# Kernel optimization log

Measured on AMD Instinct MI355X. Metric: run time of the kernel, lower is better.

The kernel has to match this reference:

```python
import jax, jax.numpy as jnp
import numpy as np

THRESH = 64.0        # titans.surprise_threshold
NOISE_SCALE = 1e-6   # tie-breaking noise scale in _update_memory


def setup_inputs() -> dict:
    key = jax.random.key(0)
    ks = jax.random.split(key, 8)
    B, S, H, M = 2, 2048, 1024, 8192
    return {
        "hidden_states": jax.random.normal(ks[0], (B, S, H), dtype=jnp.float32),
        "memory_buffer": jax.random.normal(ks[1], (M, H), dtype=jnp.float32),
        "importance_scores": jax.random.uniform(ks[2], (M,), dtype=jnp.float32),
        "Wq": jax.random.normal(ks[3], (H, H), dtype=jnp.float32) * 0.02,
        "bq": jnp.zeros((H,), dtype=jnp.float32),
        "Wk": jax.random.normal(ks[4], (H, H), dtype=jnp.float32) * 0.02,
        "bk": jnp.zeros((H,), dtype=jnp.float32),
        "noise": jax.random.normal(ks[5], (M,), dtype=jnp.float32),
    }


def reference(hidden_states, memory_buffer, importance_scores, Wq, bq, Wk, bk, noise):
    B, S, H = hidden_states.shape
    M = memory_buffer.shape[0]

    # ---- surprise (gradient_norm method) ----
    # proxy_loss = sum((h - 0)^2)  =>  d loss / d h = 2h  =>  surprise = 2*||h||_2
    cands = hidden_states.reshape(-1, H)                      # [B*S, H]
    surprise = 2.0 * jnp.linalg.norm(cands, axis=-1)          # [B*S]

    # ---- _update_memory (torch.no_grad) ----
    # mask below-threshold candidates out, then take the (at most memory_size)
    # most surprising candidates in descending order (== argsort descending +
    # slice in the torch code; -inf entries sort last and are marked invalid).
    K = min(cands.shape[0], M)
    masked = jnp.where(surprise > THRESH, surprise, -jnp.inf)
    top_s, top_i = jax.lax.top_k(masked, K)                   # descending surprise
    valid = top_s > THRESH                                    # true only for real candidates

    # least-important memory slots (topk largest=False with tie-break noise)
    _, least_idx = jax.lax.top_k(-(importance_scores + noise * NOISE_SCALE), K)

    # scatter-write: i-th most surprising candidate -> i-th least important slot.
    # invalid lanes write to index M which is dropped (out of range).
    write_idx = jnp.where(valid, least_idx, M)                # [K]
    states_w = jax.lax.stop_gradient(cands[top_i])            # update path is no_grad
    scores_w = jax.lax.stop_gradient(jnp.where(valid, top_s, 0.0))
    new_buffer = memory_buffer.at[write_idx].set(states_w, mode="drop")   # [M, H]
    new_importance = importance_scores.at[write_idx].set(scores_w, mode="drop")
    del new_importance  # bookkeeping state; does not affect retrieved output

    # ---- query (cross-attention over memory) ----
    q = hidden_states @ Wq.T + bq                             # [B, S, H]
    mk = new_buffer @ Wk.T + bk                               # [M, H]
    scores = jnp.einsum("bsh,mh->bsm", q, mk) * (H ** -0.5)
    attn = jax.nn.softmax(scores, axis=-1)                    # [B, S, M]
    retrieved = jnp.einsum("bsm,mh->bsh", attn, new_buffer)   # [B, S, H]
    return retrieved
```

## Files before the change

### kernel.cpp

```cpp
#include <hip/hip_runtime.h>
#include <hip/hip_bf16.h>
#include <math.h>
#include <stdint.h>

typedef __attribute__((ext_vector_type(4))) float floatx4;
typedef __attribute__((ext_vector_type(8))) short shortx8;
typedef __attribute__((ext_vector_type(4))) unsigned short ushortx4;

#define BS_CAND 4096
#define HDIM    1024
#define MSLOTS  8192
#define THRESH  64.0f
#define PV_SPLIT 4
#define PS_COLS 128

__device__ __forceinline__ unsigned short f2b_bits(float f) {
    __hip_bfloat16 b = __float2bfloat16(f);
    return *(unsigned short*)&b;
}
__device__ __forceinline__ float b2f_bits(unsigned short u) {
    return __uint_as_float(((unsigned)u) << 16);
}

__device__ __forceinline__ float blockReduceSum(float x) {
    __shared__ float red[4];
    #pragma unroll
    for (int o = 32; o > 0; o >>= 1) x += __shfl_down(x, o, 64);
    int lane = threadIdx.x & 63, w = threadIdx.x >> 6;
    if (lane == 0) red[w] = x;
    __syncthreads();
    float s = red[0] + red[1] + red[2] + red[3];
    __syncthreads();
    return s;
}

__global__ __launch_bounds__(256) void pre_k(const float* __restrict__ h,
                                             float* __restrict__ sur,
                                             __hip_bfloat16* __restrict__ Hbf,
                                             const float* __restrict__ imp,
                                             const float* __restrict__ noi,
                                             float* __restrict__ keys,
                                             int* __restrict__ row_src,
                                             const float* __restrict__ Wq,
                                             __hip_bfloat16* __restrict__ Wqbf,
                                             const float* __restrict__ Wk,
                                             __hip_bfloat16* __restrict__ Wkbf) {
    int b = blockIdx.x;
    if (b < BS_CAND) {
        float4 v = ((const float4*)(h + (size_t)b * HDIM))[threadIdx.x];
        ushortx4 o;
        o.x = f2b_bits(v.x); o.y = f2b_bits(v.y);
        o.z = f2b_bits(v.z); o.w = f2b_bits(v.w);
        ((ushortx4*)(Hbf + (size_t)b * HDIM))[threadIdx.x] = o;
        float s = v.x * v.x + v.y * v.y + v.z * v.z + v.w * v.w;
        float tot = blockReduceSum(s);
        if (threadIdx.x == 0) sur[b] = 2.0f * sqrtf(tot);
    } else if (b < BS_CAND + MSLOTS / 256) {
        int i = (b - BS_CAND) * 256 + threadIdx.x;
        keys[i] = imp[i] + noi[i] * 1e-6f;
        row_src[i] = -1;
    } else {
        int w = b - (BS_CAND + MSLOTS / 256);
        const float* in = (w < 1024) ? Wq : Wk;
        __hip_bfloat16* out = (w < 1024) ? Wqbf : Wkbf;
        int j = (w & 1023) * 256 + threadIdx.x;
        float4 v = ((const float4*)in)[j];
        ushortx4 o;
        o.x = f2b_bits(v.x); o.y = f2b_bits(v.y);
        o.z = f2b_bits(v.z); o.w = f2b_bits(v.w);
        ((ushortx4*)out)[j] = o;
    }
}

__global__ __launch_bounds__(256) void ranks_k(const float* __restrict__ sur,
                                               int* __restrict__ cand_ord,
                                               const float* __restrict__ keys,
                                               int* __restrict__ slot_ord) {
    int b = blockIdx.x;
    if (b < BS_CAND) {
        float ki = sur[b];
        float cnt = 0.f;
        for (int j = threadIdx.x; j < BS_CAND; j += 256) {
            float kj = sur[j];
            cnt += ((kj > ki) || (kj == ki && j < b)) ? 1.f : 0.f;
        }
        float r = blockReduceSum(cnt);
        if (threadIdx.x == 0) cand_ord[(int)r] = b;
    } else {
        int i = b - BS_CAND;
        float ki = keys[i];
        float cnt = 0.f;
        for (int j = threadIdx.x; j < MSLOTS; j += 256) {
            float kj = keys[j];
            cnt += ((kj < ki) || (kj == ki && j < i)) ? 1.f : 0.f;
        }
        float r = blockReduceSum(cnt);
        if (threadIdx.x == 0) slot_ord[(int)r] = i;
    }
}

__global__ __launch_bounds__(256) void scatter_k(const int* __restrict__ cand_order,
                                                 const int* __restrict__ slot_order,
                                                 const float* __restrict__ sur,
                                                 int* __restrict__ row_src) {
    int i = blockIdx.x * 256 + threadIdx.x;
    int c = cand_order[i];
    if (sur[c] > THRESH) row_src[slot_order[i]] = c;
}

__global__ __launch_bounds__(256) void bbt_k(const float* __restrict__ mem,
                                             const float* __restrict__ hid,
                                             const int* __restrict__ src,
                                             __hip_bfloat16* __restrict__ B,
                                             __hip_bfloat16* __restrict__ BT) {
    __shared__ unsigned short t[64][72];
    int cb = blockIdx.x * 64, rb = blockIdx.y * 64;
    int tx = threadIdx.x & 63, ty = threadIdx.x >> 6;
    #pragma unroll
    for (int k = 0; k < 16; k++) {
        int r = ty * 16 + k;
        int s = src[rb + r];
        const float* row = (s < 0) ? (mem + (size_t)(rb + r) * HDIM)
                                   : (hid + (size_t)s * HDIM);
        unsigned short b = f2b_bits(row[cb + tx]);
        t[r][tx] = b;
        ((unsigned short*)B)[(size_t)(rb + r) * HDIM + cb + tx] = b;
    }
    __syncthreads();
    #pragma unroll
    for (int k = 0; k < 16; k++) {
        int c = ty * 16 + k;
        ((unsigned short*)BT)[(size_t)(cb + c) * MSLOTS + rb + tx] = t[tx][c];
    }
}

__device__ __forceinline__ void load_lds16(const __hip_bfloat16* g, __hip_bfloat16* l) {
    __builtin_amdgcn_global_load_lds(
        (const __attribute__((address_space(1))) void*)g,
        (__attribute__((address_space(3))) void*)l, 16, 0, 0);
}

template <int EPI, int SWAP>
__global__ __launch_bounds__(512, 2) void gemm_bt(const __hip_bfloat16* __restrict__ A,
                                                  const __hip_bfloat16* __restrict__ Bt,
                                                  const __hip_bfloat16* __restrict__ Bt2,
                                                  __hip_bfloat16* __restrict__ outH,
                                                  const float* __restrict__ bias,
                                                  const float* __restrict__ bias2,
                                                  float* __restrict__ ps,
                                                  int rows0b,
                                                  int M, int N, int K, int ksplit,
                                                  float scale) {
    extern __shared__ char lds[];
    const int tid = threadIdx.x;
    const int wave = tid >> 6, lane = tid & 63;
    const int lm = lane & 15, lq = lane >> 4;
    const int wm = wave >> 2, wn = wave & 3;
    const int bm = SWAP ? blockIdx.x : blockIdx.y;
    const int bn = SWAP ? blockIdx.y : blockIdx.x;
    const int kb = blockIdx.z * ksplit;
    const int niters = ksplit >> 7;

    const __hip_bfloat16* BtSel = (EPI == 1 && bm >= rows0b) ? Bt2 : Bt;
    const float* biasSel = (EPI == 1 && bm >= rows0b) ? bias2 : bias;

    const int l8 = lane >> 3;
    const int colsrc = ((((lane & 7) << 4) ^ (l8 << 4)) >> 1);
    const __hip_bfloat16* Abase = A + (size_t)bm * 256 * K;
    const __hip_bfloat16* Bbase = BtSel + (size_t)bn * 256 * K;
    const __hip_bfloat16* srcA[2][2];
    const __hip_bfloat16* srcB[2][2];
    #pragma unroll
    for (int h = 0; h < 2; h++)
        #pragma unroll
        for (int t = 0; t < 2; t++) {
            int row = t * 128 + h * 64 + wave * 8 + l8;
            srcA[h][t] = Abase + (size_t)row * K + colsrc;
            srcB[h][t] = Bbase + (size_t)row * K + colsrc;
        }

    const int cxor = (lq << 4) ^ ((lm & 7) << 4);
    const int a_b0 = (wm * 64 + lm) * 128 + cxor;
    const int a_b1 = a_b0 ^ 64;
    const int b_b0 = (wn * 32 + lm) * 128 + cxor;
    const int b_b1 = b_b0 ^ 64;

    floatx4 acc[8][4];
    #pragma unroll
    for (int i = 0; i < 8; i++)
        #pragma unroll
        for (int j = 0; j < 4; j++) acc[i][j] = {0.f, 0.f, 0.f, 0.f};

    shortx8 af[4][2], bf0h[2][2], bf1h[2][2];

#define LDSV(off) (*(const shortx8*)(lds + (off)))
#define READ_A(g, bo) do {                                                  \
    const int ab_ = (bo) + (g) * 16384;                                     \
    af[0][0] = LDSV(ab_ + a_b0);        af[0][1] = LDSV(ab_ + a_b1);        \
    af[1][0] = LDSV(ab_ + a_b0 + 2048); af[1][1] = LDSV(ab_ + a_b1 + 2048); \
    af[2][0] = LDSV(ab_ + a_b0 + 4096); af[2][1] = LDSV(ab_ + a_b1 + 4096); \
    af[3][0] = LDSV(ab_ + a_b0 + 6144); af[3][1] = LDSV(ab_ + a_b1 + 6144); \
} while (0)
#define READ_B(dst, g, bo) do {                                             \
    const int bb_ = (bo) + 32768 + (g) * 16384;                             \
    dst[0][0] = LDSV(bb_ + b_b0);        dst[0][1] = LDSV(bb_ + b_b1);      \
    dst[1][0] = LDSV(bb_ + b_b0 + 2048); dst[1][1] = LDSV(bb_ + b_b1 + 2048);\
} while (0)
#define STAGE(xs, h, buf, kofs) do {                                        \
    char* d_ = lds + (buf) * 65536 + (xs) * 32768 + (h) * 16384 + wave * 1024; \
    load_lds16(((xs) ? srcB : srcA)[h][0] + (kofs), (__hip_bfloat16*)d_);   \
    load_lds16(((xs) ? srcB : srcA)[h][1] + (kofs), (__hip_bfloat16*)(d_ + 8192)); \
} while (0)
#define MFQ(mh, nh, BF) do {                                                \
    __builtin_amdgcn_s_setprio(1);                                          \
    _Pragma("unroll")                                                       \
    for (int ii_ = 0; ii_ < 4; ii_++)                                       \
        _Pragma("unroll")                                                   \
        for (int jj_ = 0; jj_ < 2; jj_++) {                                 \
            acc[(mh)*4+ii_][(nh)*2+jj_] = __builtin_amdgcn_mfma_f32_16x16x32_bf16( \
                af[ii_][0], BF[jj_][0], acc[(mh)*4+ii_][(nh)*2+jj_], 0, 0, 0); \
            acc[(mh)*4+ii_][(nh)*2+jj_] = __builtin_amdgcn_mfma_f32_16x16x32_bf16( \
                af[ii_][1], BF[jj_][1], acc[(mh)*4+ii_][(nh)*2+jj_], 0, 0, 0); \
        }                                                                   \
    __builtin_amdgcn_s_setprio(0);                                          \
} while (0)
#define BAR() __builtin_amdgcn_s_barrier()
#define LGKM0() asm volatile("s_waitcnt lgkmcnt(0)" ::: "memory")
#define VMC6() asm volatile("s_waitcnt vmcnt(6)" ::: "memory")
#define VMC0() asm volatile("s_waitcnt vmcnt(0)" ::: "memory")

    STAGE(0, 0, 0, kb);
    STAGE(1, 1, 0, kb);
    STAGE(0, 1, 0, kb);
    STAGE(1, 0, 0, kb);
    STAGE(0, 0, 1, kb + 64);
    STAGE(1, 1, 1, kb + 64);
    STAGE(0, 1, 1, kb + 64);
    VMC6();
    BAR();

#define ITER(E, kcur, knext) do {                                           \
                                                                   \
    READ_A(0, 0); READ_B(bf0h, 0, 0); STAGE(1, 0, 1, (kcur) + 64);          \
    BAR(); LGKM0(); MFQ(0, 0, bf0h); BAR();                                 \
                                                                   \
    READ_B(bf1h, 1, 0); if (E) STAGE(0, 0, 0, (knext));                     \
    BAR(); LGKM0(); MFQ(0, 1, bf1h); BAR();                                 \
                                                                   \
    READ_A(1, 0); if (E) STAGE(1, 1, 0, (knext));                           \
    BAR(); LGKM0(); MFQ(1, 1, bf1h); BAR();                                 \
                                     \
    if (E) { STAGE(0, 1, 0, (knext)); VMC6(); } else { VMC0(); }            \
    BAR(); LGKM0(); MFQ(1, 0, bf0h); BAR();                                 \
                                                                   \
    READ_A(0, 65536); READ_B(bf0h, 0, 65536); if (E) STAGE(1, 0, 0, (knext)); \
    BAR(); LGKM0(); MFQ(0, 0, bf0h); BAR();                                 \
                                                                   \
    READ_B(bf1h, 1, 65536); if (E) STAGE(0, 0, 1, (knext) + 64);            \
    BAR(); LGKM0(); MFQ(0, 1, bf1h); BAR();                                 \
                                                                   \
    READ_A(1, 65536); if (E) STAGE(1, 1, 1, (knext) + 64);                  \
    BAR(); LGKM0(); MFQ(1, 1, bf1h); BAR();                                 \
                                                         \
    if (E) { STAGE(0, 1, 1, (knext) + 64); VMC6(); }                        \
    BAR(); LGKM0(); MFQ(1, 0, bf0h); BAR();                                 \
} while (0)

    int it = 0;
    #pragma unroll 1
    for (; it < niters - 1; ++it) {
        const int kc = kb + it * 128;
        ITER(1, kc, kc + 128);
    }
    {
        const int kc = kb + it * 128;
        ITER(0, kc, 0);
    }

#undef ITER
#undef LDSV
#undef READ_A
#undef READ_B
#undef STAGE
#undef MFQ
#undef BAR
#undef LGKM0
#undef VMC6
#undef VMC0

    if (EPI == 2) {
        #pragma unroll
        for (int i = 0; i < 8; i++) {
            const int grow0 = bm * 256 + wm * 128 + (i >> 2) * 64 + (i & 3) * 16 + lq * 4;
            #pragma unroll
            for (int r = 0; r < 4; r++) {
                float rs = 0.f;
                #pragma unroll
                for (int j = 0; j < 4; j++) {
                    const int gcol = bn * 256 + (wn >> 1) * 128 + (j >> 1) * 64 +
                                     (wn & 1) * 32 + (j & 1) * 16 + lm;
                    float e = __expf(acc[i][j][r] * scale);
                    unsigned short eb = f2b_bits(e);
                    ((unsigned short*)outH)[(size_t)(grow0 + r) * N + gcol] = eb;
                    rs += b2f_bits(eb);
                }
                rs += __shfl_xor(rs, 1, 64);
                rs += __shfl_xor(rs, 2, 64);
                rs += __shfl_xor(rs, 4, 64);
                rs += __shfl_xor(rs, 8, 64);
                if (lm == 0)
                    ps[(size_t)(grow0 + r) * PS_COLS + bn * 4 + wn] = rs;
            }
        }
    } else {
        __hip_bfloat16* outHz = outH + ((EPI == 4) ? (size_t)blockIdx.z * M * N : 0);
        #pragma unroll
        for (int i = 0; i < 8; i++) {
            const int grow0 = bm * 256 + wm * 128 + (i >> 2) * 64 + (i & 3) * 16 + lq * 4;
            #pragma unroll
            for (int j = 0; j < 4; j++) {
                const int gcol = bn * 256 + (wn >> 1) * 128 + (j >> 1) * 64 +
                                 (wn & 1) * 32 + (j & 1) * 16 + lm;
                #pragma unroll
                for (int r = 0; r < 4; r++) {
                    float v = acc[i][j][r];
                    size_t idx = (size_t)(grow0 + r) * N + gcol;
                    if (EPI == 1) outHz[idx] = __float2bfloat16(v + biasSel[gcol]);
                    else          outHz[idx] = __float2bfloat16(v * scale);
                }
            }
        }
    }
}

__global__ __launch_bounds__(256) void reduce4_k(const ushortx4* __restrict__ part,
                                                 const float* __restrict__ ps,
                                                 float4* __restrict__ out) {
    int row = blockIdx.x;
    float s = 0.f;
    if (threadIdx.x < PS_COLS) s = ps[(size_t)row * PS_COLS + threadIdx.x];
    float tot = blockReduceSum(s);
    float inv = 1.f / tot;
    size_t base = (size_t)row * (HDIM / 4) + threadIdx.x;
    const size_t stride = (size_t)BS_CAND * (HDIM / 4);
    float4 o = {0.f, 0.f, 0.f, 0.f};
    #pragma unroll
    for (int z = 0; z < PV_SPLIT; z++) {
        ushortx4 p = part[base + (size_t)z * stride];
        o.x += b2f_bits(p.x); o.y += b2f_bits(p.y);
        o.z += b2f_bits(p.z); o.w += b2f_bits(p.w);
    }
    o.x *= inv; o.y *= inv; o.z *= inv; o.w *= inv;
    out[(size_t)row * (HDIM / 4) + threadIdx.x] = o;
}

extern "C" void kernel_launch(void* const* d_in, const int* in_sizes, int n_in,
                              void* d_out, int out_size, void* d_ws, size_t ws_size,
                              hipStream_t stream) {
    const float* hidden = (const float*)d_in[0];
    const float* membuf = (const float*)d_in[1];
    const float* imp    = (const float*)d_in[2];
    const float* Wq     = (const float*)d_in[3];
    const float* bq     = (const float*)d_in[4];
    const float* Wk     = (const float*)d_in[5];
    const float* bk     = (const float*)d_in[6];
    const float* noise  = (const float*)d_in[7];

    static bool s_attr = false;
    if (!s_attr) {
        (void)hipFuncSetAttribute((const void*)gemm_bt<1, 0>,
                                  hipFuncAttributeMaxDynamicSharedMemorySize, 131072);
        (void)hipFuncSetAttribute((const void*)gemm_bt<2, 0>,
                                  hipFuncAttributeMaxDynamicSharedMemorySize, 131072);
        (void)hipFuncSetAttribute((const void*)gemm_bt<4, 1>,
                                  hipFuncAttributeMaxDynamicSharedMemorySize, 131072);
        s_attr = true;
    }

    char* ws = (char*)d_ws;
    size_t off = 0;
    auto alloc = [&](size_t bytes) -> void* {
        void* p = ws + off;
        off += (bytes + 255) & ~(size_t)255;
        return p;
    };
    float*          surprise = (float*)alloc(BS_CAND * 4);
    float*          skeys    = (float*)alloc(MSLOTS * 4);
    float*          ps       = (float*)alloc((size_t)BS_CAND * PS_COLS * 4);
    int*            cand_ord = (int*)alloc(BS_CAND * 4);
    int*            slot_ord = (int*)alloc(MSLOTS * 4);
    int*            row_src  = (int*)alloc(MSLOTS * 4);
    __hip_bfloat16* Wqbf = (__hip_bfloat16*)alloc((size_t)HDIM * HDIM * 2);
    __hip_bfloat16* Wkbf = (__hip_bfloat16*)alloc((size_t)HDIM * HDIM * 2);
    __hip_bfloat16* BbfT = (__hip_bfloat16*)alloc((size_t)HDIM * MSLOTS * 2);
    size_t s_base = off;
    __hip_bfloat16* Sbf = (__hip_bfloat16*)(ws + s_base);
    __hip_bfloat16* Hbf = (__hip_bfloat16*)(ws + s_base);
    __hip_bfloat16* Bbf = (__hip_bfloat16*)(ws + s_base + (size_t)BS_CAND * HDIM * 2);
    off = s_base + ((size_t)BS_CAND * MSLOTS * 2 + 255) & ~(size_t)255;
    size_t t_base = off;
    __hip_bfloat16* qbf  = (__hip_bfloat16*)alloc((size_t)BS_CAND * HDIM * 2);
    __hip_bfloat16* mkbf = (__hip_bfloat16*)alloc((size_t)MSLOTS * HDIM * 2);
    __hip_bfloat16* part = (__hip_bfloat16*)(ws + t_base);

    pre_k<<<BS_CAND + MSLOTS / 256 + 2048, 256, 0, stream>>>(
        hidden, surprise, Hbf, imp, noise, skeys, row_src, Wq, Wqbf, Wk, Wkbf);
    ranks_k<<<BS_CAND + MSLOTS, 256, 0, stream>>>(surprise, cand_ord, skeys, slot_ord);
    scatter_k<<<BS_CAND / 256, 256, 0, stream>>>(cand_ord, slot_ord, surprise, row_src);
    bbt_k<<<dim3(HDIM / 64, MSLOTS / 64), 256, 0, stream>>>(
        membuf, hidden, row_src, Bbf, BbfT);
    gemm_bt<1, 0><<<dim3(HDIM / 256, (BS_CAND + MSLOTS) / 256), 512, 131072, stream>>>(
        Hbf, Wqbf, Wkbf, qbf, bq, bk, nullptr, BS_CAND / 256,
        BS_CAND + MSLOTS, HDIM, HDIM, HDIM, 1.f);
    gemm_bt<2, 0><<<dim3(MSLOTS / 256, BS_CAND / 256), 512, 131072, stream>>>(
        qbf, mkbf, nullptr, Sbf, nullptr, nullptr, ps, 1 << 30,
        BS_CAND, MSLOTS, HDIM, HDIM, 0.03125f);
    gemm_bt<4, 1><<<dim3(BS_CAND / 256, HDIM / 256, PV_SPLIT), 512, 131072, stream>>>(
        Sbf, BbfT, nullptr, part, nullptr, nullptr, nullptr, 1 << 30,
        BS_CAND, HDIM, MSLOTS, MSLOTS / PV_SPLIT, 1.f);
    reduce4_k<<<BS_CAND, 256, 0, stream>>>((const ushortx4*)part, ps, (float4*)d_out);
}
```

Baseline: 312.5 us.

## Double-buffer LDS fragment registers to overlap LDS reads with MFMA

Splits the A and B fragment registers into double buffers and issues LDS reads for the next MFMA quadrant before the current one runs. Partial lgkmcnt waits replace full drains, so LDS read latency can hide behind matrix math, and the first fragments of each half-iteration are prefetched across the barrier. The cost is extra VGPR pressure, which could lower occupancy or cause spills, and a more fragile wait-count schedule.

```diff
diff --git a/kernel.cpp b/kernel.cpp
--- a/kernel.cpp
+++ b/kernel.cpp
@@ -191,15 +191,16 @@
         #pragma unroll
         for (int j = 0; j < 4; j++) acc[i][j] = {0.f, 0.f, 0.f, 0.f};
 
-    shortx8 af[4][2], bf0h[2][2], bf1h[2][2];
+    shortx8 afX[4][2], afY[4][2];
+    shortx8 bQ0[2][2], bQ1[2][2], bR0[2][2];
 
 #define LDSV(off) (*(const shortx8*)(lds + (off)))
-#define READ_A(g, bo) do {                                                  \
+#define READ_A(dst, g, bo) do {                                             \
     const int ab_ = (bo) + (g) * 16384;                                     \
-    af[0][0] = LDSV(ab_ + a_b0);        af[0][1] = LDSV(ab_ + a_b1);        \
-    af[1][0] = LDSV(ab_ + a_b0 + 2048); af[1][1] = LDSV(ab_ + a_b1 + 2048); \
-    af[2][0] = LDSV(ab_ + a_b0 + 4096); af[2][1] = LDSV(ab_ + a_b1 + 4096); \
-    af[3][0] = LDSV(ab_ + a_b0 + 6144); af[3][1] = LDSV(ab_ + a_b1 + 6144); \
+    dst[0][0] = LDSV(ab_ + a_b0);        dst[0][1] = LDSV(ab_ + a_b1);      \
+    dst[1][0] = LDSV(ab_ + a_b0 + 2048); dst[1][1] = LDSV(ab_ + a_b1 + 2048);\
+    dst[2][0] = LDSV(ab_ + a_b0 + 4096); dst[2][1] = LDSV(ab_ + a_b1 + 4096);\
+    dst[3][0] = LDSV(ab_ + a_b0 + 6144); dst[3][1] = LDSV(ab_ + a_b1 + 6144);\
 } while (0)
 #define READ_B(dst, g, bo) do {                                             \
     const int bb_ = (bo) + 32768 + (g) * 16384;                             \
@@ -211,21 +212,24 @@
     load_lds16(((xs) ? srcB : srcA)[h][0] + (kofs), (__hip_bfloat16*)d_);   \
     load_lds16(((xs) ? srcB : srcA)[h][1] + (kofs), (__hip_bfloat16*)(d_ + 8192)); \
 } while (0)
-#define MFQ(mh, nh, BF) do {                                                \
+#define MFQ(mh, nh, AF, BF) do {                                            \
     __builtin_amdgcn_s_setprio(1);                                          \
     _Pragma("unroll")                                                       \
     for (int ii_ = 0; ii_ < 4; ii_++)                                       \
         _Pragma("unroll")                                                   \
         for (int jj_ = 0; jj_ < 2; jj_++) {                                 \
             acc[(mh)*4+ii_][(nh)*2+jj_] = __builtin_amdgcn_mfma_f32_16x16x32_bf16( \
-                af[ii_][0], BF[jj_][0], acc[(mh)*4+ii_][(nh)*2+jj_], 0, 0, 0); \
+                AF[ii_][0], BF[jj_][0], acc[(mh)*4+ii_][(nh)*2+jj_], 0, 0, 0); \
             acc[(mh)*4+ii_][(nh)*2+jj_] = __builtin_amdgcn_mfma_f32_16x16x32_bf16( \
-                af[ii_][1], BF[jj_][1], acc[(mh)*4+ii_][(nh)*2+jj_], 0, 0, 0); \
+                AF[ii_][1], BF[jj_][1], acc[(mh)*4+ii_][(nh)*2+jj_], 0, 0, 0); \
         }                                                                   \
     __builtin_amdgcn_s_setprio(0);                                          \
 } while (0)
 #define BAR() __builtin_amdgcn_s_barrier()
-#define LGKM0() asm volatile("s_waitcnt lgkmcnt(0)" ::: "memory")
+#define LGKM0()  asm volatile("s_waitcnt lgkmcnt(0)" ::: "memory")
+#define LGKM4()  asm volatile("s_waitcnt lgkmcnt(4)" ::: "memory")
+#define LGKM8()  asm volatile("s_waitcnt lgkmcnt(8)" ::: "memory")
+#define LGKM12() asm volatile("s_waitcnt lgkmcnt(12)" ::: "memory")
 #define VMC6() asm volatile("s_waitcnt vmcnt(6)" ::: "memory")
 #define VMC0() asm volatile("s_waitcnt vmcnt(0)" ::: "memory")
 
@@ -238,32 +242,37 @@
     STAGE(0, 1, 1, kb + 64);
     VMC6();
     BAR();
+    READ_A(afX, 0, 0); READ_B(bQ0, 0, 0);
 
 #define ITER(E, kcur, knext) do {                                           \
-                                                                   \
-    READ_A(0, 0); READ_B(bf0h, 0, 0); STAGE(1, 0, 1, (kcur) + 64);          \
-    BAR(); LGKM0(); MFQ(0, 0, bf0h); BAR();                                 \
-                                                                   \
-    READ_B(bf1h, 1, 0); if (E) STAGE(0, 0, 0, (knext));                     \
-    BAR(); LGKM0(); MFQ(0, 1, bf1h); BAR();                                 \
-                                                                   \
-    READ_A(1, 0); if (E) STAGE(1, 1, 0, (knext));                           \
-    BAR(); LGKM0(); MFQ(1, 1, bf1h); BAR();                                 \
-                                     \
+      \
+    READ_B(bQ1, 1, 0); STAGE(1, 0, 1, (kcur) + 64);                         \
+    BAR(); LGKM4(); MFQ(0, 0, afX, bQ0); BAR();                             \
+                                             \
+    READ_A(afY, 1, 0); if (E) STAGE(0, 0, 0, (knext));                      \
+    BAR(); LGKM8(); MFQ(0, 1, afX, bQ1); BAR();                             \
+                                                         \
+    if (E) STAGE(1, 1, 0, (knext));                                         \
+    BAR(); LGKM0(); MFQ(1, 1, afY, bQ1); BAR();                             \
+                                         \
     if (E) { STAGE(0, 1, 0, (knext)); VMC6(); } else { VMC0(); }            \
-    BAR(); LGKM0(); MFQ(1, 0, bf0h); BAR();                                 \
-                                                                   \
-    READ_A(0, 65536); READ_B(bf0h, 0, 65536); if (E) STAGE(1, 0, 0, (knext)); \
-    BAR(); LGKM0(); MFQ(0, 0, bf0h); BAR();                                 \
-                                                                   \
-    READ_B(bf1h, 1, 65536); if (E) STAGE(0, 0, 1, (knext) + 64);            \
-    BAR(); LGKM0(); MFQ(0, 1, bf1h); BAR();                                 \
-                                                                   \
-    READ_A(1, 65536); if (E) STAGE(1, 1, 1, (knext) + 64);                  \
-    BAR(); LGKM0(); MFQ(1, 1, bf1h); BAR();                                 \
+    BAR(); READ_A(afX, 0, 65536); READ_B(bR0, 0, 65536); LGKM12();          \
+    MFQ(1, 0, afY, bQ0); BAR();                                             \
+                                             \
+    READ_B(bQ1, 1, 65536); if (E) STAGE(1, 0, 0, (knext));                  \
+    BAR(); LGKM4(); MFQ(0, 0, afX, bR0); BAR();                             \
+                                             \
+    READ_A(afY, 1, 65536); if (E) STAGE(0, 0, 1, (knext) + 64);             \
+    BAR(); LGKM8(); MFQ(0, 1, afX, bQ1); BAR();                             \
                                                          \
+    if (E) STAGE(1, 1, 1, (knext) + 64);                                    \
+    BAR(); LGKM0(); MFQ(1, 1, afY, bQ1); BAR();                             \
+      \
     if (E) { STAGE(0, 1, 1, (knext) + 64); VMC6(); }                        \
-    BAR(); LGKM0(); MFQ(1, 0, bf0h); BAR();                                 \
+    BAR();                                                                  \
+    if (E) { READ_A(afX, 0, 0); READ_B(bQ0, 0, 0); LGKM12(); }              \
+    else   { LGKM0(); }                                                     \
+    MFQ(1, 0, afY, bR0); BAR();                                             \
 } while (0)
 
     int it = 0;
@@ -285,6 +294,9 @@
 #undef MFQ
 #undef BAR
 #undef LGKM0
+#undef LGKM4
+#undef LGKM8
+#undef LGKM12
 #undef VMC6
 #undef VMC0
 
```

After: 649.6 us. 2.08x slower.

## Restructure GEMM main loop into four phases with fewer barriers

Applied to the files above, without the earlier changes.

Regroups the 8-phase ping-pong main loop of the bf16 MFMA GEMM into 4 phases. Each phase issues two MFMA quadrants back to back and reorders the global-to-LDS staging, adjusting the vmcnt waits (a new vmcnt(4)) to match. The goal is to halve the number of barrier and lgkmcnt synchronisation points per K-iteration and give the matrix cores longer uninterrupted runs. In exchange, LDS reads and global loads overlap less finely with compute, and a mistake in the wait counts could create races.

```diff
diff --git a/kernel.cpp b/kernel.cpp
--- a/kernel.cpp
+++ b/kernel.cpp
@@ -227,43 +227,38 @@
 #define BAR() __builtin_amdgcn_s_barrier()
 #define LGKM0() asm volatile("s_waitcnt lgkmcnt(0)" ::: "memory")
 #define VMC6() asm volatile("s_waitcnt vmcnt(6)" ::: "memory")
+#define VMC4() asm volatile("s_waitcnt vmcnt(4)" ::: "memory")
 #define VMC0() asm volatile("s_waitcnt vmcnt(0)" ::: "memory")
 
     STAGE(0, 0, 0, kb);
+    STAGE(1, 0, 0, kb);
     STAGE(1, 1, 0, kb);
     STAGE(0, 1, 0, kb);
-    STAGE(1, 0, 0, kb);
     STAGE(0, 0, 1, kb + 64);
+    STAGE(1, 0, 1, kb + 64);
     STAGE(1, 1, 1, kb + 64);
-    STAGE(0, 1, 1, kb + 64);
     VMC6();
     BAR();
 
 #define ITER(E, kcur, knext) do {                                           \
-                                                                   \
-    READ_A(0, 0); READ_B(bf0h, 0, 0); STAGE(1, 0, 1, (kcur) + 64);          \
-    BAR(); LGKM0(); MFQ(0, 0, bf0h); BAR();                                 \
-                                                                   \
-    READ_B(bf1h, 1, 0); if (E) STAGE(0, 0, 0, (knext));                     \
-    BAR(); LGKM0(); MFQ(0, 1, bf1h); BAR();                                 \
-                                                                   \
-    READ_A(1, 0); if (E) STAGE(1, 1, 0, (knext));                           \
-    BAR(); LGKM0(); MFQ(1, 1, bf1h); BAR();                                 \
-                                     \
-    if (E) { STAGE(0, 1, 0, (knext)); VMC6(); } else { VMC0(); }            \
-    BAR(); LGKM0(); MFQ(1, 0, bf0h); BAR();                                 \
-                                                                   \
-    READ_A(0, 65536); READ_B(bf0h, 0, 65536); if (E) STAGE(1, 0, 0, (knext)); \
-    BAR(); LGKM0(); MFQ(0, 0, bf0h); BAR();                                 \
-                                                                   \
-    READ_B(bf1h, 1, 65536); if (E) STAGE(0, 0, 1, (knext) + 64);            \
-    BAR(); LGKM0(); MFQ(0, 1, bf1h); BAR();                                 \
-                                                                   \
-    READ_A(1, 65536); if (E) STAGE(1, 1, 1, (knext) + 64);                  \
-    BAR(); LGKM0(); MFQ(1, 1, bf1h); BAR();                                 \
-                                                         \
-    if (E) { STAGE(0, 1, 1, (knext) + 64); VMC6(); }                        \
-    BAR(); LGKM0(); MFQ(1, 0, bf0h); BAR();                                 \
+                        \
+    READ_A(0, 0); READ_B(bf0h, 0, 0); READ_B(bf1h, 1, 0);                   \
+    STAGE(0, 1, 1, (kcur) + 64);                                            \
+    BAR(); LGKM0(); MFQ(0, 0, bf0h); MFQ(0, 1, bf1h); BAR();                \
+         \
+    READ_A(1, 0);                                                           \
+    if (E) { STAGE(0, 0, 0, (knext)); STAGE(1, 0, 0, (knext)); VMC4(); }    \
+    else   { VMC0(); }                                                      \
+    BAR(); LGKM0(); MFQ(1, 1, bf1h); MFQ(1, 0, bf0h); BAR();                \
+                      \
+    READ_A(0, 65536); READ_B(bf0h, 0, 65536); READ_B(bf1h, 1, 65536);       \
+    if (E) { STAGE(1, 1, 0, (knext)); STAGE(0, 1, 0, (knext)); }            \
+    BAR(); LGKM0(); MFQ(0, 0, bf0h); MFQ(0, 1, bf1h); BAR();                \
+      \
+    READ_A(1, 65536);                                                       \
+    if (E) { STAGE(0, 0, 1, (knext) + 64); STAGE(1, 0, 1, (knext) + 64);    \
+             STAGE(1, 1, 1, (knext) + 64); VMC6(); }                        \
+    BAR(); LGKM0(); MFQ(1, 1, bf1h); MFQ(1, 0, bf0h); BAR();                \
 } while (0)
 
     int it = 0;
@@ -286,6 +281,7 @@
 #undef BAR
 #undef LGKM0
 #undef VMC6
+#undef VMC4
 #undef VMC0
 
     if (EPI == 2) {
```

New measurement: 315.1 us. Within noise of the previous version (+0.8%).
